# Kernel optimization log

Measured on AMD Instinct MI355X. Metric: run time of the kernel, lower is better.

Reference implementation:

```python
import jax, jax.numpy as jnp
import numpy as np

DIM = 64
KSIZE = 3
BN_EPS = 1e-5

def _bn(x):
    # eval-mode BatchNorm2d with default running stats (mean=0, var=1) and affine (1, 0)
    return x / jnp.sqrt(1.0 + BN_EPS)

def _downsample(x, params):
    # four stride-2 3x3 convs: 3 -> 8 -> 16 -> 32 -> 64, BN after each, GELU except after last
    for i, (w, b) in enumerate(params):
        x = jax.lax.conv_general_dilated(x, w, (2, 2), ((1, 1), (1, 1))) + b[None, :, None, None]
        x = _bn(x)
        if i < 3:
            x = jax.nn.gelu(x, approximate=False)
    return x

def _attn(dx, q, kw, kb, vw, vb, pw, pb, dw, db):
    # single-head cross attention: learned queries q (1,T,C) attend to dx (B,N,C)
    scale = DIM ** -0.5
    k = dx @ kw.T + kb
    v = dx @ vw.T + vb
    a = jax.nn.softmax((q @ jnp.swapaxes(k, -1, -2)) * scale, axis=-1)  # (B,T,N)
    o = (a @ v) @ pw.T + pb                                            # (B,T,C)
    return o @ dw.T + db                                               # (B,T,1)

def _gk1d(sigma):
    half = (KSIZE - 1) * 0.5
    x = jnp.linspace(-half, half, KSIZE)
    pdf = jnp.exp(-0.5 * (x / sigma) ** 2)
    return pdf / pdf.sum()

def _gain_denoise(I1, r1, r2, gain, sigma):
    # per-image gain + gaussian-blur unsharp masking, vectorized over the batch
    def one(img, r1i, r2i, gi, si):
        ig = gi * img                                       # (3,H,W)
        k2 = _gk1d(r2i)[:, None] * _gk1d(r1i)[None, :]      # (k,k), sigma_x=r1, sigma_y=r2
        kern = jnp.broadcast_to(k2, (3, 1, KSIZE, KSIZE))   # depthwise kernel
        p = KSIZE // 2
        xp = jnp.pad(ig[None], ((0, 0), (0, 0), (p, p), (p, p)), mode='reflect')
        blur = jax.lax.conv_general_dilated(xp, kern, (1, 1), 'VALID', feature_group_count=3)[0]
        return blur + si * (img - blur)
    return jax.vmap(one)(I1, r1, r2, gain, sigma)

def setup_inputs():
    key = jax.random.key(0)
    ks = iter(jax.random.split(key, 64))
    def rn(shape, s=0.05):
        return jax.random.normal(next(ks), shape, dtype=jnp.float32) * s
    def ru(shape):
        return jax.random.uniform(next(ks), shape, dtype=jnp.float32)
    inp = {"I1": ru((8, 3, 512, 512))}
    for pre, T in (("kp", 4), ("mp", 10)):
        inp[pre + "_q"] = ru((1, T, DIM))
        chans = [3, DIM // 8, DIM // 4, DIM // 2, DIM]
        for i in range(4):
            inp[pre + "_c%dw" % (i + 1)] = rn((chans[i + 1], chans[i], 3, 3), 0.1)
            inp[pre + "_c%db" % (i + 1)] = jnp.zeros((chans[i + 1],), jnp.float32)
        for nm, shp in (("kw", (DIM, DIM)), ("vw", (DIM, DIM)), ("pw", (DIM, DIM)), ("dw", (1, DIM))):
            inp[pre + "_" + nm] = rn(shp)
        for nm, n in (("kb", DIM), ("vb", DIM), ("pb", DIM), ("db", 1)):
            inp[pre + "_" + nm] = jnp.zeros((n,), jnp.float32)
    inp["kp_gain_base"] = jnp.ones((1,), jnp.float32)  # mode='normal'
    dims = [3, 32, 32, 32, 32, 3]
    for i in range(5):
        inp["lut_w%d" % i] = rn((dims[i + 1], dims[i]), 0.2)
        inp["lut_b%d" % i] = jnp.zeros((dims[i + 1],), jnp.float32)
    return inp

def reference(I1, kp_q, kp_c1w, kp_c1b, kp_c2w, kp_c2b, kp_c3w, kp_c3b, kp_c4w, kp_c4b,
              kp_kw, kp_kb, kp_vw, kp_vb, kp_pw, kp_pb, kp_dw, kp_db, kp_gain_base,
              mp_q, mp_c1w, mp_c1b, mp_c2w, mp_c2b, mp_c3w, mp_c3b, mp_c4w, mp_c4b,
              mp_kw, mp_kb, mp_vw, mp_vb, mp_pw, mp_pb, mp_dw, mp_db,
              lut_w0, lut_b0, lut_w1, lut_b1, lut_w2, lut_b2, lut_w3, lut_b3, lut_w4, lut_b4):
    B = I1.shape[0]
    # --- Kernel_Predictor ---
    dx = _downsample(I1, [(kp_c1w, kp_c1b), (kp_c2w, kp_c2b), (kp_c3w, kp_c3b), (kp_c4w, kp_c4b)])
    dx = dx.reshape(B, DIM, -1).transpose(0, 2, 1)            # (B,N,C), N=(H/16)*(W/16)
    o = _attn(dx, kp_q, kp_kw, kp_kb, kp_vw, kp_vb, kp_pw, kp_pb, kp_dw, kp_db)[..., 0]  # (B,4)
    r1 = 0.1 * o[:, 0] + 3.0
    r2 = 0.1 * o[:, 1] + 2.0
    gain = o[:, 2] + kp_gain_base[0]
    sigma = jax.nn.sigmoid(o[:, 3])
    # --- gain + gaussian unsharp denoise ---
    I2 = jnp.clip(_gain_denoise(I1, r1, r2, gain, sigma), 1e-5, 1.0)
    # --- Matrix_Predictor ---
    dx2 = _downsample(I2, [(mp_c1w, mp_c1b), (mp_c2w, mp_c2b), (mp_c3w, mp_c3b), (mp_c4w, mp_c4b)])
    dx2 = dx2.reshape(B, DIM, -1).transpose(0, 2, 1)
    o2 = _attn(dx2, mp_q, mp_kw, mp_kb, mp_vw, mp_vb, mp_pw, mp_pb, mp_dw, mp_db)  # (B,10,1)
    ccm = 0.1 * o2[:, :9, 0].reshape(B, 3, 3) + jnp.eye(3, dtype=I1.dtype)
    dist = jax.nn.relu(o2[:, 9, 0]) + 1.0                     # (B,)
    # --- Shades-of-Gray white balance + CCM ---
    hwc = I2.transpose(0, 2, 3, 1)                            # (B,H,W,3)
    imgP = hwc ** dist[:, None, None, None]
    ch = jnp.mean(imgP, axis=(1, 2)) ** (1.0 / dist)[:, None]  # (B,3)
    avg = jnp.mean(imgP, axis=(1, 2, 3)) ** (1.0 / dist)       # (B,)
    I3 = hwc / (ch / avg[:, None])[:, None, None, :]
    I4 = jnp.clip(jnp.einsum('bhwc,bdc->bhwd', I3, ccm), 1e-5, 1.0)
    # --- NILUT residual per-pixel MLP ---
    h = jax.nn.relu(I4 @ lut_w0.T + lut_b0)
    h = jnp.tanh(h @ lut_w1.T + lut_b1)
    h = jnp.tanh(h @ lut_w2.T + lut_b2)
    h = jnp.tanh(h @ lut_w3.T + lut_b3)
    I5 = jnp.clip(h @ lut_w4.T + lut_b4 + I4, 0.0, 1.0)
    return I5.transpose(0, 3, 1, 2)                           # (B,3,H,W)
```

## Files before the change

kernel.cpp:

```cpp
#include <hip/hip_runtime.h>
#include <math.h>


#define BN_MUL 0.9999950000374997f

static constexpr int BB   = 8;
static constexpr int HH   = 512;
static constexpr int WW   = 512;
static constexpr int HW   = HH * WW;
static constexpr int NTOK = 1024;
static constexpr int DIMC = 64;
static constexpr int WBCH = 32;

typedef _Float16 f16x8 __attribute__((ext_vector_type(8)));
typedef _Float16 f16x2 __attribute__((ext_vector_type(2)));
typedef float    f32x4 __attribute__((ext_vector_type(4)));

__device__ __forceinline__ float gelu_exact(float x) {
    return 0.5f * x * (1.0f + erff(x * 0.7071067811865476f));
}

template<int Cin, int Hin, int OCT, bool GELU>
__global__ __launch_bounds__(256) void conv_s2(const float* __restrict__ in,
                                               const float* __restrict__ wt,
                                               const float* __restrict__ bs,
                                               float* __restrict__ out)
{
    constexpr int Win  = Hin, Hout = Hin / 2, Wout = Hin / 2;
    constexpr int WSH  = (Wout == 256) ? 8 : (Wout == 128) ? 7 : (Wout == 64) ? 6 : 5;
    constexpr int PLANE = Hout * Wout;

    const int sp  = blockIdx.x * 256 + threadIdx.x;
    const int ow  = sp & (Wout - 1);
    const int oh  = sp >> WSH;
    const int oc0 = blockIdx.y * OCT;
    const int b   = blockIdx.z;
    const int Cout = (int)gridDim.y * OCT;

    float acc[OCT];
    #pragma unroll
    for (int o = 0; o < OCT; ++o) acc[o] = bs[oc0 + o];

    const int ih0 = oh * 2 - 1, iw0 = ow * 2 - 1;
    const float fh0 = (ih0 >= 0) ? 1.f : 0.f;
    const float fw0 = (iw0 >= 0) ? 1.f : 0.f;
    const int r0 = (ih0 >= 0) ? ih0 : 0;
    const int cc0 = (iw0 >= 0) ? iw0 : 0;

    const float* ip = in + (size_t)(b * Cin) * Hin * Win;
    #pragma unroll
    for (int ic = 0; ic < Cin; ++ic) {
        const float* pl = ip + ic * Hin * Win;
        const float* p0 = pl + r0 * Win;
        const float* p1 = pl + (ih0 + 1) * Win;
        const float* p2 = pl + (ih0 + 2) * Win;
        float  v00 = p0[cc0] * (fh0 * fw0);
        float2 va  = *(const float2*)(p0 + iw0 + 1);
        float  v01 = va.x * fh0, v02 = va.y * fh0;
        float  v10 = p1[cc0] * fw0;
        float2 vb  = *(const float2*)(p1 + iw0 + 1);
        float  v20 = p2[cc0] * fw0;
        float2 vc  = *(const float2*)(p2 + iw0 + 1);
        #pragma unroll
        for (int o = 0; o < OCT; ++o) {
            const float* wr = wt + ((oc0 + o) * Cin + ic) * 9;
            acc[o] += v00 * wr[0] + v01 * wr[1] + v02 * wr[2]
                    + v10 * wr[3] + vb.x * wr[4] + vb.y * wr[5]
                    + v20 * wr[6] + vc.x * wr[7] + vc.y * wr[8];
        }
    }
    #pragma unroll
    for (int o = 0; o < OCT; ++o) {
        float a = acc[o] * BN_MUL;
        if (GELU) a = gelu_exact(a);
        out[(size_t)(b * Cout + oc0 + o) * PLANE + sp] = a;
    }
}

__global__ __launch_bounds__(256) void denoise_conv1_kernel(
    const float* __restrict__ I1, const float* __restrict__ attno,
    const float* __restrict__ gain_base,
    const float* __restrict__ wt, const float* __restrict__ bs,
    float* __restrict__ I2, float* __restrict__ out)
{
    const int sp = blockIdx.x * 256 + threadIdx.x;
    const int ow = sp & 255;
    const int oh = sp >> 8;
    const int b  = blockIdx.z;

    const float o0 = attno[b * 4 + 0], o1 = attno[b * 4 + 1];
    const float o2 = attno[b * 4 + 2], o3 = attno[b * 4 + 3];
    const float r1 = 0.1f * o0 + 3.0f;
    const float r2 = 0.1f * o1 + 2.0f;
    const float g  = o2 + gain_base[0];
    const float sg = 1.0f / (1.0f + __expf(-o3));
    const float ex = __expf(-0.5f / (r1 * r1));
    const float nx = 1.0f / (2.0f * ex + 1.0f);
    const float ey = __expf(-0.5f / (r2 * r2));
    const float ny = 1.0f / (2.0f * ey + 1.0f);
    const float kx0 = ex * nx, kx1 = nx;
    const float ky0 = ey * ny, ky1 = ny;

    const int rbase = 2 * oh - 2, cbase = 2 * ow - 2;
    int ri[5], ci[5];
    #pragma unroll
    for (int i = 0; i < 5; ++i) {
        int r = rbase + i; ri[i] = r < 0 ? -r : (r > 511 ? 1022 - r : r);
        int c = cbase + i; ci[i] = c < 0 ? -c : (c > 511 ? 1022 - c : c);
    }
    const bool topE = (oh == 0), leftE = (ow == 0);

    float acc[8];
    #pragma unroll
    for (int o = 0; o < 8; ++o) acc[o] = bs[o];

    #pragma unroll
    for (int c = 0; c < 3; ++c) {
        const float* ip = I1 + ((size_t)b * 3 + c) * HW;
        float p[5][5];
        #pragma unroll
        for (int i = 0; i < 5; ++i) {
            const float* rp = ip + ri[i] * WW;
            #pragma unroll
            for (int j = 0; j < 5; ++j) p[i][j] = rp[ci[j]];
        }
        float hs[5][3];
        #pragma unroll
        for (int i = 0; i < 5; ++i)
            #pragma unroll
            for (int j = 0; j < 3; ++j)
                hs[i][j] = kx0 * (p[i][j] + p[i][j + 2]) + kx1 * p[i][j + 1];
        float w2[3][3];
        #pragma unroll
        for (int i = 0; i < 3; ++i)
            #pragma unroll
            for (int j = 0; j < 3; ++j) {
                float bl = g * (ky0 * (hs[i][j] + hs[i + 2][j]) + ky1 * hs[i + 1][j]);
                float val = bl + sg * (p[i + 1][j + 1] - bl);
                w2[i][j] = fminf(fmaxf(val, 1e-5f), 1.0f);
            }
        float* op = I2 + ((size_t)b * 3 + c) * HW + (2 * oh) * WW + 2 * ow;
        float2 w0v; w0v.x = w2[1][1]; w0v.y = w2[1][2];
        float2 w1v; w1v.x = w2[2][1]; w1v.y = w2[2][2];
        *(float2*)op        = w0v;
        *(float2*)(op + WW) = w1v;
        if (topE)  { w2[0][0] = 0.f; w2[0][1] = 0.f; w2[0][2] = 0.f; }
        if (leftE) { w2[0][0] = 0.f; w2[1][0] = 0.f; w2[2][0] = 0.f; }
        #pragma unroll
        for (int o = 0; o < 8; ++o) {
            const float* wr = wt + (o * 3 + c) * 9;
            acc[o] += w2[0][0] * wr[0] + w2[0][1] * wr[1] + w2[0][2] * wr[2]
                    + w2[1][0] * wr[3] + w2[1][1] * wr[4] + w2[1][2] * wr[5]
                    + w2[2][0] * wr[6] + w2[2][1] * wr[7] + w2[2][2] * wr[8];
        }
    }
    #pragma unroll
    for (int o = 0; o < 8; ++o)
        out[(b * 8 + o) * 65536 + sp] = gelu_exact(acc[o] * BN_MUL);
}

__global__ __launch_bounds__(1024) void attn_kernel(
    const float* __restrict__ dx, const float* __restrict__ q,
    const float* __restrict__ kw, const float* __restrict__ kb,
    const float* __restrict__ vw, const float* __restrict__ vb,
    const float* __restrict__ pw, const float* __restrict__ pb,
    const float* __restrict__ dw, const float* __restrict__ db,
    float* __restrict__ outv, int T)
{
    __shared__ float qk[DIMC];
    __shared__ float sc[NTOK];
    __shared__ float wredm[16];
    __shared__ float wreds[16];
    __shared__ float uN[DIMC];
    __shared__ float osh[DIMC];
    __shared__ float psh[DIMC];
    __shared__ float qkb_s;
    const int tid  = threadIdx.x;
    const int lane = tid & 63;
    const int wv   = tid >> 6;
    const int bt   = blockIdx.x;
    const int b = bt / T, t = bt - b * T;
    const float* qt = q + t * DIMC;

    if (tid < DIMC) {
        float s = 0.f;
        #pragma unroll
        for (int c = 0; c < DIMC; ++c) s += qt[c] * kw[c * DIMC + tid];
        qk[tid] = s;
    }
    if (tid == 1023) {
        float s = 0.f;
        #pragma unroll
        for (int c = 0; c < DIMC; ++c) s += qt[c] * kb[c];
        qkb_s = s;
    }
    __syncthreads();

    const float* dp = dx + (size_t)(b * DIMC) * NTOK;
    float s = qkb_s;
    #pragma unroll
    for (int c = 0; c < DIMC; ++c) s += qk[c] * dp[c * NTOK + tid];
    s *= 0.125f;

    float m = s;
    #pragma unroll
    for (int off = 32; off > 0; off >>= 1) m = fmaxf(m, __shfl_xor(m, off));
    if (lane == 0) wredm[wv] = m;
    __syncthreads();
    m = wredm[0];
    #pragma unroll
    for (int k = 1; k < 16; ++k) m = fmaxf(m, wredm[k]);

    float e = __expf(s - m);
    sc[tid] = e;
    float ss = e;
    #pragma unroll
    for (int off = 32; off > 0; off >>= 1) ss += __shfl_xor(ss, off);
    if (lane == 0) wreds[wv] = ss;
    __syncthreads();
    float Ssum = wreds[0];
    #pragma unroll
    for (int k = 1; k < 16; ++k) Ssum += wreds[k];

    #pragma unroll
    for (int cc = 0; cc < 4; ++cc) {
        const int c = wv * 4 + cc;
        const float* dr = dp + c * NTOK;
        float p = 0.f;
        #pragma unroll
        for (int k = 0; k < 16; ++k) p += sc[k * 64 + lane] * dr[k * 64 + lane];
        #pragma unroll
        for (int off = 32; off > 0; off >>= 1) p += __shfl_xor(p, off);
        if (lane == 0) uN[c] = p / Ssum;
    }
    __syncthreads();

    if (tid < DIMC) {
        float o = vb[tid];
        const float* vr = vw + tid * DIMC;
        #pragma unroll
        for (int cc = 0; cc < DIMC; ++cc) o += vr[cc] * uN[cc];
        osh[tid] = o;
    }
    __syncthreads();
    if (tid < DIMC) {
        float p = pb[tid];
        const float* pr = pw + tid * DIMC;
        #pragma unroll
        for (int cc = 0; cc < DIMC; ++cc) p += pr[cc] * osh[cc];
        psh[tid] = p;
    }
    __syncthreads();
    if (tid == 0) {
        float r = db[0];
        #pragma unroll
        for (int cc = 0; cc < DIMC; ++cc) r += psh[cc] * dw[cc];
        outv[bt] = r;
    }
}

__global__ __launch_bounds__(256) void wb_reduce_kernel(const float* __restrict__ I2,
                                                        const float* __restrict__ attno,
                                                        float* __restrict__ part)
{
    __shared__ float red[256];
    const int bc = blockIdx.y;
    const int b  = bc / 3;
    float d = attno[b * 10 + 9];
    d = fmaxf(d, 0.f) + 1.0f;
    constexpr int CHUNK = HW / WBCH;
    const float4* base = (const float4*)(I2 + (size_t)bc * HW + blockIdx.x * CHUNK);
    float l = 0.f;
    #pragma unroll
    for (int i = threadIdx.x, it = 0; it < CHUNK / 4 / 256; ++it, i += 256) {
        float4 v = base[i];
        l += __expf(d * __logf(v.x)) + __expf(d * __logf(v.y))
           + __expf(d * __logf(v.z)) + __expf(d * __logf(v.w));
    }
    red[threadIdx.x] = l;
    __syncthreads();
    for (int off = 128; off > 0; off >>= 1) {
        if (threadIdx.x < off) red[threadIdx.x] += red[threadIdx.x + off];
        __syncthreads();
    }
    if (threadIdx.x == 0) part[bc * WBCH + blockIdx.x] = red[0];
}

__global__ void wb_finalize_kernel(const float* __restrict__ part,
                                   const float* __restrict__ attno,
                                   float* __restrict__ wbsc,
                                   const float* __restrict__ w1,
                                   const float* __restrict__ w2,
                                   const float* __restrict__ w3,
                                   _Float16* __restrict__ whf)
{
    const int t = threadIdx.x;
    for (int i = t; i < 1024; i += 256) {
        whf[i]        = (_Float16)w1[i];
        whf[1024 + i] = (_Float16)w2[i];
        whf[2048 + i] = (_Float16)w3[i];
    }
    if (t < BB) {
        const int b = t;
        float d = attno[b * 10 + 9];
        d = fmaxf(d, 0.f) + 1.0f;
        float inv = 1.0f / d;
        float s[3];
        #pragma unroll
        for (int c = 0; c < 3; ++c) {
            float t0 = 0.f;
            const float* pp = part + (b * 3 + c) * WBCH;
            #pragma unroll
            for (int k = 0; k < WBCH; ++k) t0 += pp[k];
            s[c] = t0;
        }
        float avg = powf((s[0] + s[1] + s[2]) / (3.0f * (float)HW), inv);
        #pragma unroll
        for (int c = 0; c < 3; ++c)
            wbsc[b * 4 + c] = avg / powf(s[c] / (float)HW, inv);
    }
}

__global__ void __launch_bounds__(256) final_kernel(
    float* __restrict__ io,
    const float* __restrict__ wbsc, const float* __restrict__ attno,
    const _Float16* __restrict__ whf,
    const float* __restrict__ w0, const float* __restrict__ b0,
    const float* __restrict__ b1, const float* __restrict__ b2,
    const float* __restrict__ b3,
    const float* __restrict__ w4, const float* __restrict__ b4)
{
    constexpr int ROW = 40;
    __shared__ __align__(16) _Float16 LDS[4][64 * ROW];
    const int tid  = threadIdx.x;
    const int wv   = tid >> 6;
    const int lane = tid & 63;
    const int nn   = lane & 15;
    const int quad = lane >> 4;
    _Float16* Wl = LDS[wv];

    const int b   = blockIdx.x >> 10;
    const int pix = (blockIdx.x * 256 + tid) & (HW - 1);
    float* base = io + b * 3 * HW + pix;

    const float s0 = wbsc[b * 4 + 0], s1 = wbsc[b * 4 + 1], s2 = wbsc[b * 4 + 2];
    float v0 = base[0] * s0;
    float v1 = base[HW] * s1;
    float v2 = base[2 * HW] * s2;
    const float* o2p = attno + b * 10;
    float I4[3];
    #pragma unroll
    for (int d = 0; d < 3; ++d) {
        float m0 = 0.1f * o2p[d * 3]     + (d == 0 ? 1.f : 0.f);
        float m1 = 0.1f * o2p[d * 3 + 1] + (d == 1 ? 1.f : 0.f);
        float m2 = 0.1f * o2p[d * 3 + 2] + (d == 2 ? 1.f : 0.f);
        I4[d] = fminf(fmaxf(m0 * v0 + m1 * v1 + m2 * v2, 1e-5f), 1.0f);
    }

    #pragma unroll
    for (int j = 0; j < 32; j += 2) {
        float a0 = b0[j]   + w0[j*3]     * I4[0] + w0[j*3+1]     * I4[1] + w0[j*3+2]     * I4[2];
        float a1 = b0[j+1] + w0[(j+1)*3] * I4[0] + w0[(j+1)*3+1] * I4[1] + w0[(j+1)*3+2] * I4[2];
        f16x2 p;
        p[0] = (_Float16)fmaxf(a0, 0.f);
        p[1] = (_Float16)fmaxf(a1, 0.f);
        *(f16x2*)&Wl[lane * ROW + j] = p;
    }

    f16x8 wf[3][2];
    float bv[3][2];
    const float* bls[3] = { b1, b2, b3 };
    #pragma unroll
    for (int L = 0; L < 3; ++L) {
        #pragma unroll
        for (int h = 0; h < 2; ++h) {
            wf[L][h] = *(const f16x8*)&whf[L * 1024 + (16 * h + nn) * 32 + quad * 8];
            bv[L][h] = bls[L][16 * h + nn];
        }
    }
    asm volatile("s_waitcnt lgkmcnt(0)" ::: "memory");
    __builtin_amdgcn_sched_barrier(0);

    #pragma unroll
    for (int L = 0; L < 3; ++L) {
        f16x8 af[4];
        #pragma unroll
        for (int t = 0; t < 4; ++t)
            af[t] = *(const f16x8*)&Wl[(16 * t + nn) * ROW + quad * 8];
        asm volatile("s_waitcnt lgkmcnt(0)" ::: "memory");
        __builtin_amdgcn_sched_barrier(0);
        #pragma unroll
        for (int h = 0; h < 2; ++h) {
            f32x4 cb;
            cb[0] = cb[1] = cb[2] = cb[3] = bv[L][h];
            #pragma unroll
            for (int t = 0; t < 4; ++t) {
                f32x4 d = __builtin_amdgcn_mfma_f32_16x16x32_f16(af[t], wf[L][h], cb, 0, 0, 0);
                float a0 = __builtin_amdgcn_exp2f(d[0] * 2.8853900817779268f) + 1.0f;
                float a1 = __builtin_amdgcn_exp2f(d[1] * 2.8853900817779268f) + 1.0f;
                float a2 = __builtin_amdgcn_exp2f(d[2] * 2.8853900817779268f) + 1.0f;
                float a3 = __builtin_amdgcn_exp2f(d[3] * 2.8853900817779268f) + 1.0f;
                float p01 = a0 * a1, p23 = a2 * a3;
                float R   = __builtin_amdgcn_rcpf(p01 * p23);
                float r01 = R * p23, r23 = R * p01;
                Wl[(16 * t + quad * 4 + 0) * ROW + 16 * h + nn] = (_Float16)fmaf(-2.0f, r01 * a1, 1.0f);
                Wl[(16 * t + quad * 4 + 1) * ROW + 16 * h + nn] = (_Float16)fmaf(-2.0f, r01 * a0, 1.0f);
                Wl[(16 * t + quad * 4 + 2) * ROW + 16 * h + nn] = (_Float16)fmaf(-2.0f, r23 * a3, 1.0f);
                Wl[(16 * t + quad * 4 + 3) * ROW + 16 * h + nn] = (_Float16)fmaf(-2.0f, r23 * a2, 1.0f);
            }
        }
        asm volatile("s_waitcnt lgkmcnt(0)" ::: "memory");
        __builtin_amdgcn_sched_barrier(0);
    }

    float h4[32];
    #pragma unroll
    for (int g = 0; g < 4; ++g) {
        f16x8 rv = *(const f16x8*)&Wl[lane * ROW + g * 8];
        #pragma unroll
        for (int i = 0; i < 8; ++i) h4[g * 8 + i] = (float)rv[i];
    }
    #pragma unroll
    for (int d = 0; d < 3; ++d) {
        float a = b4[d];
        const float* wr = w4 + d * 32;
        #pragma unroll
        for (int k = 0; k < 32; ++k) a += h4[k] * wr[k];
        a += I4[d];
        base[d * HW] = fminf(fmaxf(a, 0.f), 1.0f);
    }
}

extern "C" void kernel_launch(void* const* d_in, const int* in_sizes, int n_in,
                              void* d_out, int out_size, void* d_ws, size_t ws_size,
                              hipStream_t stream)
{
    const float* I1      = (const float*)d_in[0];
    const float* kp_q    = (const float*)d_in[1];
    const float* kp_c1w  = (const float*)d_in[2];  const float* kp_c1b = (const float*)d_in[3];
    const float* kp_c2w  = (const float*)d_in[4];  const float* kp_c2b = (const float*)d_in[5];
    const float* kp_c3w  = (const float*)d_in[6];  const float* kp_c3b = (const float*)d_in[7];
    const float* kp_c4w  = (const float*)d_in[8];  const float* kp_c4b = (const float*)d_in[9];
    const float* kp_kw   = (const float*)d_in[10]; const float* kp_vw  = (const float*)d_in[11];
    const float* kp_pw   = (const float*)d_in[12]; const float* kp_dw  = (const float*)d_in[13];
    const float* kp_kb   = (const float*)d_in[14]; const float* kp_vb  = (const float*)d_in[15];
    const float* kp_pb   = (const float*)d_in[16]; const float* kp_db  = (const float*)d_in[17];
    const float* mp_q    = (const float*)d_in[18];
    const float* mp_c1w  = (const float*)d_in[19]; const float* mp_c1b = (const float*)d_in[20];
    const float* mp_c2w  = (const float*)d_in[21]; const float* mp_c2b = (const float*)d_in[22];
    const float* mp_c3w  = (const float*)d_in[23]; const float* mp_c3b = (const float*)d_in[24];
    const float* mp_c4w  = (const float*)d_in[25]; const float* mp_c4b = (const float*)d_in[26];
    const float* mp_kw   = (const float*)d_in[27]; const float* mp_vw  = (const float*)d_in[28];
    const float* mp_pw   = (const float*)d_in[29]; const float* mp_dw  = (const float*)d_in[30];
    const float* mp_kb   = (const float*)d_in[31]; const float* mp_vb  = (const float*)d_in[32];
    const float* mp_pb   = (const float*)d_in[33]; const float* mp_db  = (const float*)d_in[34];
    const float* gainb   = (const float*)d_in[35];
    const float* lw0 = (const float*)d_in[36]; const float* lb0 = (const float*)d_in[37];
    const float* lw1 = (const float*)d_in[38]; const float* lb1 = (const float*)d_in[39];
    const float* lw2 = (const float*)d_in[40]; const float* lb2 = (const float*)d_in[41];
    const float* lw3 = (const float*)d_in[42]; const float* lb3 = (const float*)d_in[43];
    const float* lw4 = (const float*)d_in[44]; const float* lb4 = (const float*)d_in[45];

    float* ws    = (float*)d_ws;
    float* ds1   = ws;
    float* ds2   = ds1 + 8 * 8 * 256 * 256;
    float* ds3   = ds2 + 8 * 16 * 128 * 128;
    float* ds4   = ds3 + 8 * 32 * 64 * 64;
    float* attno = ds4 + 8 * 64 * 32 * 32;
    float* part  = attno + 128;
    float* wbsc  = part + 24 * WBCH;
    float* I2    = (float*)d_out;
    _Float16* whf = (_Float16*)ds1;

    conv_s2<3, 512, 8, true ><<<dim3(256, 1, BB), 256, 0, stream>>>(I1,  kp_c1w, kp_c1b, ds1);
    conv_s2<8, 256, 4, true ><<<dim3(64,  4, BB), 256, 0, stream>>>(ds1, kp_c2w, kp_c2b, ds2);
    conv_s2<16, 128, 2, true><<<dim3(16, 16, BB), 256, 0, stream>>>(ds2, kp_c3w, kp_c3b, ds3);
    conv_s2<32, 64, 2, false><<<dim3(4,  32, BB), 256, 0, stream>>>(ds3, kp_c4w, kp_c4b, ds4);
    attn_kernel<<<BB * 4, 1024, 0, stream>>>(ds4, kp_q, kp_kw, kp_kb, kp_vw, kp_vb,
                                             kp_pw, kp_pb, kp_dw, kp_db, attno, 4);

    denoise_conv1_kernel<<<dim3(256, 1, BB), 256, 0, stream>>>(I1, attno, gainb,
                                                               mp_c1w, mp_c1b, I2, ds1);

    conv_s2<8, 256, 4, true ><<<dim3(64,  4, BB), 256, 0, stream>>>(ds1, mp_c2w, mp_c2b, ds2);
    conv_s2<16, 128, 2, true><<<dim3(16, 16, BB), 256, 0, stream>>>(ds2, mp_c3w, mp_c3b, ds3);
    conv_s2<32, 64, 2, false><<<dim3(4,  32, BB), 256, 0, stream>>>(ds3, mp_c4w, mp_c4b, ds4);
    attn_kernel<<<BB * 10, 1024, 0, stream>>>(ds4, mp_q, mp_kw, mp_kb, mp_vw, mp_vb,
                                              mp_pw, mp_pb, mp_dw, mp_db, attno, 10);

    wb_reduce_kernel<<<dim3(WBCH, 24), 256, 0, stream>>>(I2, attno, part);
    wb_finalize_kernel<<<1, 256, 0, stream>>>(part, attno, wbsc, lw1, lw2, lw3, whf);

    final_kernel<<<BB * HW / 256, 256, 0, stream>>>(I2, wbsc, attno, whf,
        lw0, lb0, lb1, lb2, lb3, lw4, lb4);
}
```

Measured before the change: 430.0 us.

## Fuse conv layers 2-4 into one tiled kernel and merge WB finalize into reduce

Replaces the three separate stride-2 conv launches (layers 2, 3, 4) with one kernel per image tile. Each block computes a halo'd layer-2 tile and a layer-3 tile in shared memory, then writes the layer-4 output, so the ds2/ds3 intermediates never go through global memory. The white-balance finalize step moves into the last block of the reduce kernel, found through an atomic counter, which removes one launch. In exchange the fused kernel recomputes halo pixels and leaves most threads idle in the later stages. The counter is never reset and relies on the modulo-768 test to pick the last block.

```diff
diff --git a/kernel.cpp b/kernel.cpp
--- a/kernel.cpp
+++ b/kernel.cpp
@@ -74,6 +74,125 @@
         float a = acc[o] * BN_MUL;
         if (GELU) a = gelu_exact(a);
         out[(size_t)(b * Cout + oc0 + o) * PLANE + sp] = a;
+    }
+}
+
+__global__ __launch_bounds__(256) void conv234_kernel(
+    const float* __restrict__ in,
+    const float* __restrict__ w2, const float* __restrict__ b2,
+    const float* __restrict__ w3, const float* __restrict__ b3,
+    const float* __restrict__ w4, const float* __restrict__ b4,
+    float* __restrict__ out)
+{
+    __shared__ float s2[16][209];
+    __shared__ float s3[32][45];
+    const int t  = threadIdx.x;
+    const int bx = blockIdx.x;
+    const int b  = blockIdx.z;
+    const int tx = bx & 7, ty = bx >> 3;
+
+    if (t < 209) {
+        const int y2l = t / 19, x2l = t - y2l * 19;
+        const int y2 = 8 * ty - 3 + y2l;
+        const int x2 = 16 * tx - 3 + x2l;
+        if ((unsigned)y2 < 128u && (unsigned)x2 < 128u) {
+            float acc[16];
+            #pragma unroll
+            for (int o = 0; o < 16; ++o) acc[o] = b2[o];
+            const int ih0 = 2 * y2 - 1, iw0 = 2 * x2 - 1;
+            const float fh0 = (ih0 >= 0) ? 1.f : 0.f;
+            const float fw0 = (iw0 >= 0) ? 1.f : 0.f;
+            const int r0  = (ih0 >= 0) ? ih0 : 0;
+            const int cc0 = (iw0 >= 0) ? iw0 : 0;
+            const float* ip = in + (size_t)(b * 8) * 65536;
+            #pragma unroll
+            for (int ic = 0; ic < 8; ++ic) {
+                const float* pl = ip + ic * 65536;
+                const float* p0 = pl + r0 * 256;
+                const float* p1 = pl + (ih0 + 1) * 256;
+                const float* p2 = pl + (ih0 + 2) * 256;
+                float  v00 = p0[cc0] * (fh0 * fw0);
+                float2 va  = *(const float2*)(p0 + iw0 + 1);
+                float  v01 = va.x * fh0, v02 = va.y * fh0;
+                float  v10 = p1[cc0] * fw0;
+                float2 vb  = *(const float2*)(p1 + iw0 + 1);
+                float  v20 = p2[cc0] * fw0;
+                float2 vc  = *(const float2*)(p2 + iw0 + 1);
+                #pragma unroll
+                for (int o = 0; o < 16; ++o) {
+                    const float* wr = w2 + (o * 8 + ic) * 9;
+                    acc[o] += v00 * wr[0] + v01 * wr[1] + v02 * wr[2]
+                            + v10 * wr[3] + vb.x * wr[4] + vb.y * wr[5]
+                            + v20 * wr[6] + vc.x * wr[7] + vc.y * wr[8];
+                }
+            }
+            #pragma unroll
+            for (int o = 0; o < 16; ++o)
+                s2[o][t] = gelu_exact(acc[o] * BN_MUL);
+        } else {
+            #pragma unroll
+            for (int o = 0; o < 16; ++o) s2[o][t] = 0.f;
+        }
+    }
+    __syncthreads();
+
+    if (t < 180) {
+        const int px = t % 45, cg = t / 45;
+        const int y3l = px / 9, x3l = px - y3l * 9;
+        const int y3 = 4 * ty - 1 + y3l;
+        const int x3 = 8 * tx - 1 + x3l;
+        if ((unsigned)y3 < 64u && (unsigned)x3 < 64u) {
+            float acc[8];
+            #pragma unroll
+            for (int j = 0; j < 8; ++j) acc[j] = b3[cg * 8 + j];
+            #pragma unroll
+            for (int ic = 0; ic < 16; ++ic) {
+                const float* sp = &s2[ic][(2 * y3l) * 19 + 2 * x3l];
+                float v0 = sp[0],  v1 = sp[1],  v2 = sp[2];
+                float v3 = sp[19], v4 = sp[20], v5 = sp[21];
+                float v6 = sp[38], v7 = sp[39], v8 = sp[40];
+                #pragma unroll
+                for (int j = 0; j < 8; ++j) {
+                    const float* wr = w3 + ((cg * 8 + j) * 16 + ic) * 9;
+                    acc[j] += v0 * wr[0] + v1 * wr[1] + v2 * wr[2]
+                            + v3 * wr[3] + v4 * wr[4] + v5 * wr[5]
+                            + v6 * wr[6] + v7 * wr[7] + v8 * wr[8];
+                }
+            }
+            #pragma unroll
+            for (int j = 0; j < 8; ++j)
+                s3[cg * 8 + j][px] = gelu_exact(acc[j] * BN_MUL);
+        } else {
+            #pragma unroll
+            for (int j = 0; j < 8; ++j) s3[cg * 8 + j][px] = 0.f;
+        }
+    }
+    __syncthreads();
+
+    {
+        const int px = t & 7, cg = t >> 3;
+        const int y4l = px >> 2, x4l = px & 3;
+        const int y4 = 2 * ty + y4l, x4 = 4 * tx + x4l;
+        const int oc0 = cg * 2;
+        float a0 = b4[oc0], a1 = b4[oc0 + 1];
+        #pragma unroll
+        for (int ic = 0; ic < 32; ++ic) {
+            const float* sp = &s3[ic][(2 * y4l) * 9 + 2 * x4l];
+            float v0 = sp[0],  v1 = sp[1],  v2 = sp[2];
+            float v3 = sp[9],  v4 = sp[10], v5 = sp[11];
+            float v6 = sp[18], v7 = sp[19], v8 = sp[20];
+            const float* wr0 = w4 + (oc0 * 32 + ic) * 9;
+            const float* wr1 = w4 + ((oc0 + 1) * 32 + ic) * 9;
+            a0 += v0 * wr0[0] + v1 * wr0[1] + v2 * wr0[2]
+                + v3 * wr0[3] + v4 * wr0[4] + v5 * wr0[5]
+                + v6 * wr0[6] + v7 * wr0[7] + v8 * wr0[8];
+            a1 += v0 * wr1[0] + v1 * wr1[1] + v2 * wr1[2]
+                + v3 * wr1[3] + v4 * wr1[4] + v5 * wr1[5]
+                + v6 * wr1[6] + v7 * wr1[7] + v8 * wr1[8];
+        }
+        float* op = out + (size_t)(b * 64 + oc0) * 1024 + y4 * 32 + x4;
+        op[0]    = a0 * BN_MUL;
+        op[1024] = a1 * BN_MUL;
     }
 }
 
@@ -259,11 +378,15 @@
     }
 }
 
-__global__ __launch_bounds__(256) void wb_reduce_kernel(const float* __restrict__ I2,
-                                                        const float* __restrict__ attno,
-                                                        float* __restrict__ part)
+__global__ __launch_bounds__(256) void wb_reduce_kernel(
+    const float* __restrict__ I2, const float* __restrict__ attno,
+    float* __restrict__ part, unsigned* __restrict__ cnt,
+    float* __restrict__ wbsc,
+    const float* __restrict__ w1f, const float* __restrict__ w2f,
+    const float* __restrict__ w3f, _Float16* __restrict__ whf)
 {
     __shared__ float red[256];
+    __shared__ int lastf;
     const int bc = blockIdx.y;
     const int b  = bc / 3;
     float d = attno[b * 10 + 9];
@@ -283,33 +406,32 @@
         if (threadIdx.x < off) red[threadIdx.x] += red[threadIdx.x + off];
         __syncthreads();
     }
-    if (threadIdx.x == 0) part[bc * WBCH + blockIdx.x] = red[0];
-}
-
-__global__ void wb_finalize_kernel(const float* __restrict__ part,
-                                   const float* __restrict__ attno,
-                                   float* __restrict__ wbsc,
-                                   const float* __restrict__ w1,
-                                   const float* __restrict__ w2,
-                                   const float* __restrict__ w3,
-                                   _Float16* __restrict__ whf)
-{
+    if (threadIdx.x == 0) {
+        part[bc * WBCH + blockIdx.x] = red[0];
+        __threadfence();
+        unsigned g = atomicAdd(cnt, 1u);
+        lastf = ((g % 768u) == 767u) ? 1 : 0;
+    }
+    __syncthreads();
+    if (!lastf) return;
+    __threadfence();
+
     const int t = threadIdx.x;
     for (int i = t; i < 1024; i += 256) {
-        whf[i]        = (_Float16)w1[i];
-        whf[1024 + i] = (_Float16)w2[i];
-        whf[2048 + i] = (_Float16)w3[i];
+        whf[i]        = (_Float16)w1f[i];
+        whf[1024 + i] = (_Float16)w2f[i];
+        whf[2048 + i] = (_Float16)w3f[i];
     }
     if (t < BB) {
-        const int b = t;
-        float d = attno[b * 10 + 9];
-        d = fmaxf(d, 0.f) + 1.0f;
-        float inv = 1.0f / d;
+        const int bb = t;
+        float dd = attno[bb * 10 + 9];
+        dd = fmaxf(dd, 0.f) + 1.0f;
+        float inv = 1.0f / dd;
         float s[3];
         #pragma unroll
         for (int c = 0; c < 3; ++c) {
             float t0 = 0.f;
-            const float* pp = part + (b * 3 + c) * WBCH;
+            const float* pp = part + (bb * 3 + c) * WBCH;
             #pragma unroll
             for (int k = 0; k < WBCH; ++k) t0 += pp[k];
             s[c] = t0;
@@ -317,7 +439,7 @@
         float avg = powf((s[0] + s[1] + s[2]) / (3.0f * (float)HW), inv);
         #pragma unroll
         for (int c = 0; c < 3; ++c)
-            wbsc[b * 4 + c] = avg / powf(s[c] / (float)HW, inv);
+            wbsc[bb * 4 + c] = avg / powf(s[c] / (float)HW, inv);
     }
 }
 
@@ -469,27 +591,26 @@
     float* attno = ds4 + 8 * 64 * 32 * 32;
     float* part  = attno + 128;
     float* wbsc  = part + 24 * WBCH;
+    unsigned* wbcnt = (unsigned*)(wbsc + 32);
     float* I2    = (float*)d_out;
     _Float16* whf = (_Float16*)ds1;
 
-    conv_s2<3, 512, 8, true ><<<dim3(256, 1, BB), 256, 0, stream>>>(I1,  kp_c1w, kp_c1b, ds1);
-    conv_s2<8, 256, 4, true ><<<dim3(64,  4, BB), 256, 0, stream>>>(ds1, kp_c2w, kp_c2b, ds2);
-    conv_s2<16, 128, 2, true><<<dim3(16, 16, BB), 256, 0, stream>>>(ds2, kp_c3w, kp_c3b, ds3);
-    conv_s2<32, 64, 2, false><<<dim3(4,  32, BB), 256, 0, stream>>>(ds3, kp_c4w, kp_c4b, ds4);
+    conv_s2<3, 512, 8, true><<<dim3(256, 1, BB), 256, 0, stream>>>(I1, kp_c1w, kp_c1b, ds1);
+    conv234_kernel<<<dim3(128, 1, BB), 256, 0, stream>>>(ds1,
+        kp_c2w, kp_c2b, kp_c3w, kp_c3b, kp_c4w, kp_c4b, ds4);
     attn_kernel<<<BB * 4, 1024, 0, stream>>>(ds4, kp_q, kp_kw, kp_kb, kp_vw, kp_vb,
                                              kp_pw, kp_pb, kp_dw, kp_db, attno, 4);
 
     denoise_conv1_kernel<<<dim3(256, 1, BB), 256, 0, stream>>>(I1, attno, gainb,
                                                                mp_c1w, mp_c1b, I2, ds1);
 
-    conv_s2<8, 256, 4, true ><<<dim3(64,  4, BB), 256, 0, stream>>>(ds1, mp_c2w, mp_c2b, ds2);
-    conv_s2<16, 128, 2, true><<<dim3(16, 16, BB), 256, 0, stream>>>(ds2, mp_c3w, mp_c3b, ds3);
-    conv_s2<32, 64, 2, false><<<dim3(4,  32, BB), 256, 0, stream>>>(ds3, mp_c4w, mp_c4b, ds4);
+    conv234_kernel<<<dim3(128, 1, BB), 256, 0, stream>>>(ds1,
+        mp_c2w, mp_c2b, mp_c3w, mp_c3b, mp_c4w, mp_c4b, ds4);
     attn_kernel<<<BB * 10, 1024, 0, stream>>>(ds4, mp_q, mp_kw, mp_kb, mp_vw, mp_vb,
                                               mp_pw, mp_pb, mp_dw, mp_db, attno, 10);
 
-    wb_reduce_kernel<<<dim3(WBCH, 24), 256, 0, stream>>>(I2, attno, part);
-    wb_finalize_kernel<<<1, 256, 0, stream>>>(part, attno, wbsc, lw1, lw2, lw3, whf);
+    wb_reduce_kernel<<<dim3(WBCH, 24), 256, 0, stream>>>(I2, attno, part, wbcnt,
+                                                         wbsc, lw1, lw2, lw3, whf);
 
     final_kernel<<<BB * HW / 256, 256, 0, stream>>>(I2, wbsc, attno, whf,
         lw0, lb0, lb1, lb2, lb3, lw4, lb4);
```

New measurement: 1.300 ms. 3.02x slower.
